# Kernel optimization log

Hardware: AMD Instinct MI355X
Metric: run time of the kernel (lower is better)

The kernel has to match this reference:

```python
import jax, jax.numpy as jnp
import numpy as np

B, N, K = 4, 50000, 128   # batch, surface points, deformation nodes
GD = 128                  # SDF grid resolution (D=H=W)


def setup_inputs() -> dict:
    key = jax.random.key(0)
    ks = jax.random.split(key, 7)
    constants = jax.random.normal(ks[0], (B, K), dtype=jnp.float32)
    scales = 0.05 + 0.25 * jax.random.uniform(ks[1], (B, K), dtype=jnp.float32)
    # proper-ish rotations via QR of random matrices
    M = jax.random.normal(ks[2], (B, K, 3, 3), dtype=jnp.float32)
    rotations, _ = jnp.linalg.qr(M)
    centers = jax.random.uniform(ks[3], (B, K, 3), dtype=jnp.float32, minval=-0.5, maxval=0.5)
    surface_samples = jax.random.uniform(ks[4], (B, N, 6), dtype=jnp.float32, minval=-0.5, maxval=0.5)
    grid = jax.random.normal(ks[5], (B, GD, GD, GD), dtype=jnp.float32)
    # world2grid maps world [-0.5,0.5] -> grid index [0, GD-1]
    w2g = np.zeros((B, 4, 4), dtype=np.float32)
    w2g[:, 0, 0] = w2g[:, 1, 1] = w2g[:, 2, 2] = float(GD - 1)
    w2g[:, :3, 3] = float(GD - 1) / 2.0
    w2g[:, 3, 3] = 1.0
    world2grid = jnp.asarray(w2g)
    return {"constants": constants, "scales": scales, "rotations": rotations,
            "centers": centers, "surface_samples": surface_samples,
            "grid": grid, "world2grid": world2grid}


def _trilinear_border(vol, xyz):
    """torch grid_sample (5D, bilinear, align_corners=True, border) for one batch.
    vol: (D,H,W); xyz: (N,3) normalized coords in [-1,1], order (x,y,z)."""
    D, H, W = vol.shape
    x = jnp.clip((xyz[:, 0] + 1.0) * 0.5 * (W - 1), 0.0, W - 1)
    y = jnp.clip((xyz[:, 1] + 1.0) * 0.5 * (H - 1), 0.0, H - 1)
    z = jnp.clip((xyz[:, 2] + 1.0) * 0.5 * (D - 1), 0.0, D - 1)
    x0 = jnp.floor(x); y0 = jnp.floor(y); z0 = jnp.floor(z)
    fx = x - x0; fy = y - y0; fz = z - z0
    x0i = x0.astype(jnp.int32); x1i = jnp.minimum(x0i + 1, W - 1)
    y0i = y0.astype(jnp.int32); y1i = jnp.minimum(y0i + 1, H - 1)
    z0i = z0.astype(jnp.int32); z1i = jnp.minimum(z0i + 1, D - 1)
    c000 = vol[z0i, y0i, x0i]; c001 = vol[z0i, y0i, x1i]
    c010 = vol[z0i, y1i, x0i]; c011 = vol[z0i, y1i, x1i]
    c100 = vol[z1i, y0i, x0i]; c101 = vol[z1i, y0i, x1i]
    c110 = vol[z1i, y1i, x0i]; c111 = vol[z1i, y1i, x1i]
    c00 = c000 * (1 - fx) + c001 * fx
    c01 = c010 * (1 - fx) + c011 * fx
    c10 = c100 * (1 - fx) + c101 * fx
    c11 = c110 * (1 - fx) + c111 * fx
    c0 = c00 * (1 - fy) + c01 * fy
    c1 = c10 * (1 - fy) + c11 * fy
    return c0 * (1 - fz) + c1 * fz


def reference(constants, scales, rotations, centers, surface_samples, grid, world2grid):
    pts = surface_samples[..., :3]                       # (B,N,3)
    diff = pts[:, :, None, :] - centers[:, None, :, :]   # (B,N,K,3)  == p - t_source
    d2 = jnp.sum(diff * diff, axis=-1)                   # (B,N,K)
    # sample_rbf_weights with use_constants=True
    w = jnp.exp(-d2 / (2.0 * scales * scales)[:, None, :]) * (constants * constants)[:, None, :]
    w = w / jnp.sum(w, axis=-1, keepdims=True)           # normalize over nodes

    # target = roll batch by -1 (source_idx+1 mod B)
    R_t = jnp.roll(rotations, -1, axis=0)
    R_rel = jnp.einsum('bkij,bklj->bkil', R_t, rotations)       # R_target @ R_source^T
    c_t = jnp.roll(centers, -1, axis=0)
    transformed = jnp.einsum('bkij,bnkj->bnki', R_rel, diff) + c_t[:, None, :, :]
    blended = jnp.einsum('bnk,bnki->bni', w, transformed)        # (B,N,3)

    w2g_t = jnp.roll(world2grid, -1, axis=0)
    A = w2g_t[:, :3, :3]
    t = w2g_t[:, :3, 3]
    gcs = jnp.einsum('bij,bnj->bni', A, blended) + t[:, None, :]  # grid coords (x,y,z)

    D, H, W = grid.shape[1], grid.shape[2], grid.shape[3]
    denom = jnp.array([W - 1, H - 1, D - 1], dtype=gcs.dtype)
    gcs = 2.0 * (gcs / denom) - 1.0                               # normalize to [-1,1]

    grid_t = jnp.roll(grid, -1, axis=0)
    sdf = jax.vmap(_trilinear_border)(grid_t, gcs)                # (B,N)
    return jnp.sum(jnp.mean(sdf * sdf, axis=1))
```

## Files before the change

kernel.cpp:

```cpp
#include <hip/hip_runtime.h>
#include <stdint.h>

#define K_   128
#define GD_  128
#define PSTR 20
#define KPW  32

typedef float v2f __attribute__((ext_vector_type(2)));

static __device__ __forceinline__ float fast_exp2(float x) {
#if __has_builtin(__builtin_amdgcn_exp2f)
    return __builtin_amdgcn_exp2f(x);
#else
    return exp2f(x);
#endif
}

static __device__ __forceinline__ v2f vfma(v2f a, v2f b, v2f c) {
    return __builtin_elementwise_fma(a, b, c);
}
static __device__ __forceinline__ v2f vfma_s(float a, v2f b, v2f c) {
    return __builtin_elementwise_fma((v2f)(a), b, c);
}

__global__ void surf_param_kernel(
    const float* __restrict__ constants,
    const float* __restrict__ scales,
    const float* __restrict__ rotations,
    const float* __restrict__ centers,
    const float* __restrict__ w2g,
    float* __restrict__ params,
    float* __restrict__ out,
    int B)
{
    int idx = blockIdx.x * blockDim.x + threadIdx.x;
    if (idx == 0) out[0] = 0.0f;
    if (idx >= B * K_) return;
    int b = idx / K_, k = idx - b * K_;
    int bn = (b + 1 == B) ? 0 : (b + 1);
    const float L2E = 1.4426950408889634f;

    const float* R  = rotations + (size_t)(b  * K_ + k) * 9;
    const float* Rt = rotations + (size_t)(bn * K_ + k) * 9;
    float m[9];
#pragma unroll
    for (int i = 0; i < 3; ++i)
#pragma unroll
        for (int l = 0; l < 3; ++l)
            m[i * 3 + l] = Rt[i * 3 + 0] * R[l * 3 + 0]
                         + Rt[i * 3 + 1] * R[l * 3 + 1]
                         + Rt[i * 3 + 2] * R[l * 3 + 2];

    const float* Aw = w2g + (size_t)bn * 16;
    float G[9], A[9] = {Aw[0], Aw[1], Aw[2], Aw[4], Aw[5], Aw[6], Aw[8], Aw[9], Aw[10]};
    float T[3] = {Aw[3], Aw[7], Aw[11]};
#pragma unroll
    for (int i = 0; i < 3; ++i)
#pragma unroll
        for (int l = 0; l < 3; ++l)
            G[i * 3 + l] = A[i * 3 + 0] * m[0 * 3 + l]
                         + A[i * 3 + 1] * m[1 * 3 + l]
                         + A[i * 3 + 2] * m[2 * 3 + l];

    const float* c  = centers + (size_t)(b  * K_ + k) * 3;
    const float* ct = centers + (size_t)(bn * K_ + k) * 3;
    float c0 = c[0], c1 = c[1], c2 = c[2];
    float vw0 = ct[0] - (m[0] * c0 + m[1] * c1 + m[2] * c2);
    float vw1 = ct[1] - (m[3] * c0 + m[4] * c1 + m[5] * c2);
    float vw2 = ct[2] - (m[6] * c0 + m[7] * c1 + m[8] * c2);
    float v0 = A[0] * vw0 + A[1] * vw1 + A[2] * vw2 + T[0];
    float v1 = A[3] * vw0 + A[4] * vw1 + A[5] * vw2 + T[1];
    float v2 = A[6] * vw0 + A[7] * vw1 + A[8] * vw2 + T[2];

    float sig = scales[b * K_ + k];
    float s   = 1.0f / (2.0f * sig * sig);
    float con = constants[b * K_ + k];
    float s2n = -s * L2E;
    float r   = log2f(con * con) + s2n * (c0 * c0 + c1 * c1 + c2 * c2);

    float* o = params + (size_t)idx * PSTR;
    o[0] = G[0]; o[1] = G[1]; o[2] = G[2]; o[3] = G[3];
    o[4] = G[4]; o[5] = G[5]; o[6] = G[6]; o[7] = G[7];
    o[8] = G[8]; o[9] = v0;  o[10] = v1;  o[11] = v2;
    o[12] = -2.0f * s2n * c0;
    o[13] = -2.0f * s2n * c1;
    o[14] = -2.0f * s2n * c2;
    o[15] = r;
    o[16] = s2n;
    o[17] = 0.f; o[18] = 0.f; o[19] = 0.f;
}

__global__ __launch_bounds__(256) void surf_loss_kernel(
    const float* __restrict__ sp,
    const float* __restrict__ grid,
    const float* __restrict__ params,
    float* __restrict__ out,
    int N, int B, int bpb)
{
    __shared__ float4 lds_part[4 * 4 * 64];
    __shared__ float  red[4];

    const int tid  = threadIdx.x;
    const int lane = tid & 63;
    const int wave = tid >> 6;
    const int blk  = blockIdx.x;
    const int b    = blk / bpb;
    const int base = (blk - b * bpb) * 256;
    const int bn   = (b + 1 == B) ? 0 : (b + 1);

    v2f px2[2], py2[2], pz2[2], pq2[2];
    v2f ax2[2], ay2[2], az2[2], aw2[2];
    const float* spb = sp + (size_t)b * N * 6;
#pragma unroll
    for (int j = 0; j < 4; ++j) {
        int n = base + j * 64 + lane;
        int nn = (n < N) ? n : 0;
        const float* q = spb + (size_t)nn * 6;
        float x = q[0], y = q[1], z = q[2];
        px2[j >> 1][j & 1] = x;
        py2[j >> 1][j & 1] = y;
        pz2[j >> 1][j & 1] = z;
        pq2[j >> 1][j & 1] = x * x + y * y + z * z;
    }
#pragma unroll
    for (int g = 0; g < 2; ++g) {
        ax2[g] = (v2f)0.f; ay2[g] = (v2f)0.f; az2[g] = (v2f)0.f; aw2[g] = (v2f)0.f;
    }

    const int k0 = __builtin_amdgcn_readfirstlane(wave * KPW);
    const float* __restrict__ pb = params + (size_t)b * K_ * PSTR + (size_t)k0 * PSTR;

#pragma unroll 2
    for (int kk = 0; kk < KPW; ++kk) {
        const float* pk = pb + kk * PSTR;
        const float4 f0 = *(const float4*)(pk + 0);
        const float4 f1 = *(const float4*)(pk + 4);
        const float4 f2 = *(const float4*)(pk + 8);
        const float4 f3 = *(const float4*)(pk + 12);
        const float  s2 = pk[16];
#pragma unroll
        for (int g = 0; g < 2; ++g) {
            v2f e = vfma_s(s2, pq2[g],
                    vfma_s(f3.z, pz2[g],
                    vfma_s(f3.y, py2[g],
                    vfma_s(f3.x, px2[g], (v2f)(f3.w)))));
            v2f w2;
            w2.x = fast_exp2(e.x);
            w2.y = fast_exp2(e.y);
            v2f tx = vfma_s(f0.x, px2[g],
                     vfma_s(f0.y, py2[g],
                     vfma_s(f0.z, pz2[g], (v2f)(f2.y))));
            v2f ty = vfma_s(f0.w, px2[g],
                     vfma_s(f1.x, py2[g],
                     vfma_s(f1.y, pz2[g], (v2f)(f2.z))));
            v2f tz = vfma_s(f1.z, px2[g],
                     vfma_s(f1.w, py2[g],
                     vfma_s(f2.x, pz2[g], (v2f)(f2.w))));
            ax2[g] = vfma(w2, tx, ax2[g]);
            ay2[g] = vfma(w2, ty, ay2[g]);
            az2[g] = vfma(w2, tz, az2[g]);
            aw2[g] += w2;
        }
    }

#pragma unroll
    for (int j = 0; j < 4; ++j)
        lds_part[((wave * 4 + j) << 6) + lane] =
            make_float4(ax2[j >> 1][j & 1], ay2[j >> 1][j & 1],
                        az2[j >> 1][j & 1], aw2[j >> 1][j & 1]);
    __syncthreads();

    float accum = 0.0f;
    {
        int n = base + wave * 64 + lane;
        if (n < N) {
            float sx = 0.f, sy = 0.f, sz = 0.f, sw = 0.f;
#pragma unroll
            for (int w = 0; w < 4; ++w) {
                float4 t = lds_part[((w * 4 + wave) << 6) + lane];
                sx += t.x; sy += t.y; sz += t.z; sw += t.w;
            }
            float inv = 1.0f / sw;
            float x = fminf(fmaxf(sx * inv, 0.0f), (float)(GD_ - 1));
            float y = fminf(fmaxf(sy * inv, 0.0f), (float)(GD_ - 1));
            float z = fminf(fmaxf(sz * inv, 0.0f), (float)(GD_ - 1));
            float x0f = floorf(x), y0f = floorf(y), z0f = floorf(z);
            float fx = x - x0f, fy = y - y0f, fz = z - z0f;
            int x0 = (int)x0f, y0 = (int)y0f, z0 = (int)z0f;
            int x1 = x0 + 1 > GD_ - 1 ? GD_ - 1 : x0 + 1;
            int y1 = y0 + 1 > GD_ - 1 ? GD_ - 1 : y0 + 1;
            int z1 = z0 + 1 > GD_ - 1 ? GD_ - 1 : z0 + 1;
            const float* gb = grid + (size_t)bn * GD_ * GD_ * GD_;
            int zy00 = (z0 * GD_ + y0) * GD_;
            int zy01 = (z0 * GD_ + y1) * GD_;
            int zy10 = (z1 * GD_ + y0) * GD_;
            int zy11 = (z1 * GD_ + y1) * GD_;
            float c000 = gb[zy00 + x0], c001 = gb[zy00 + x1];
            float c010 = gb[zy01 + x0], c011 = gb[zy01 + x1];
            float c100 = gb[zy10 + x0], c101 = gb[zy10 + x1];
            float c110 = gb[zy11 + x0], c111 = gb[zy11 + x1];
            float ofx = 1.0f - fx, ofy = 1.0f - fy, ofz = 1.0f - fz;
            float c00 = c000 * ofx + c001 * fx;
            float c01 = c010 * ofx + c011 * fx;
            float c10 = c100 * ofx + c101 * fx;
            float c11 = c110 * ofx + c111 * fx;
            float c0 = c00 * ofy + c01 * fy;
            float c1 = c10 * ofy + c11 * fy;
            float sdf = c0 * ofz + c1 * fz;
            accum = sdf * sdf;
        }
    }

#pragma unroll
    for (int off = 32; off > 0; off >>= 1)
        accum += __shfl_down(accum, off, 64);
    if (lane == 0) red[wave] = accum;
    __syncthreads();
    if (tid == 0)
        atomicAdd(out, (red[0] + red[1] + red[2] + red[3]) * (1.0f / (float)N));
}

extern "C" void kernel_launch(void* const* d_in, const int* in_sizes, int n_in,
                              void* d_out, int out_size, void* d_ws, size_t ws_size,
                              hipStream_t stream) {
    const float* constants = (const float*)d_in[0];
    const float* scales    = (const float*)d_in[1];
    const float* rotations = (const float*)d_in[2];
    const float* centers   = (const float*)d_in[3];
    const float* sp        = (const float*)d_in[4];
    const float* grid      = (const float*)d_in[5];
    const float* w2g       = (const float*)d_in[6];
    float* out = (float*)d_out;
    float* params = (float*)d_ws;

    const int B = in_sizes[6] / 16;
    const int N = in_sizes[4] / (6 * B);

    int np = B * K_;
    hipLaunchKernelGGL(surf_param_kernel, dim3((np + 255) / 256), dim3(256), 0, stream,
                       constants, scales, rotations, centers, w2g, params, out, B);

    const int bpb = (N + 255) / 256;
    hipLaunchKernelGGL(surf_loss_kernel, dim3(B * bpb), dim3(256), 0, stream,
                       sp, grid, params, out, N, B, bpb);
}
```

Baseline: 111.3 us.

## Fuse per-node parameter precompute into loss kernel via shared memory

Removes the separate parameter kernel and global workspace. Each block of the loss kernel now computes the 128 node parameters for its batch into LDS, then reads them from LDS in the inner loop. A tiny kernel zeroes the output. This trades a kernel launch and a global round trip for redundant per-block recomputation (about 782 blocks) and an extra barrier. Parameter reads also move from scalar or broadcast global loads to LDS loads.

```diff
diff --git a/kernel.cpp b/kernel.cpp
--- a/kernel.cpp
+++ b/kernel.cpp
@@ -23,80 +23,20 @@
     return __builtin_elementwise_fma((v2f)(a), b, c);
 }
 
-__global__ void surf_param_kernel(
+__global__ void zero_out_kernel(float* __restrict__ out) { out[0] = 0.0f; }
+
+__global__ __launch_bounds__(256) void surf_fused_kernel(
     const float* __restrict__ constants,
     const float* __restrict__ scales,
     const float* __restrict__ rotations,
     const float* __restrict__ centers,
-    const float* __restrict__ w2g,
-    float* __restrict__ params,
-    float* __restrict__ out,
-    int B)
-{
-    int idx = blockIdx.x * blockDim.x + threadIdx.x;
-    if (idx == 0) out[0] = 0.0f;
-    if (idx >= B * K_) return;
-    int b = idx / K_, k = idx - b * K_;
-    int bn = (b + 1 == B) ? 0 : (b + 1);
-    const float L2E = 1.4426950408889634f;
-
-    const float* R  = rotations + (size_t)(b  * K_ + k) * 9;
-    const float* Rt = rotations + (size_t)(bn * K_ + k) * 9;
-    float m[9];
-#pragma unroll
-    for (int i = 0; i < 3; ++i)
-#pragma unroll
-        for (int l = 0; l < 3; ++l)
-            m[i * 3 + l] = Rt[i * 3 + 0] * R[l * 3 + 0]
-                         + Rt[i * 3 + 1] * R[l * 3 + 1]
-                         + Rt[i * 3 + 2] * R[l * 3 + 2];
-
-    const float* Aw = w2g + (size_t)bn * 16;
-    float G[9], A[9] = {Aw[0], Aw[1], Aw[2], Aw[4], Aw[5], Aw[6], Aw[8], Aw[9], Aw[10]};
-    float T[3] = {Aw[3], Aw[7], Aw[11]};
-#pragma unroll
-    for (int i = 0; i < 3; ++i)
-#pragma unroll
-        for (int l = 0; l < 3; ++l)
-            G[i * 3 + l] = A[i * 3 + 0] * m[0 * 3 + l]
-                         + A[i * 3 + 1] * m[1 * 3 + l]
-                         + A[i * 3 + 2] * m[2 * 3 + l];
-
-    const float* c  = centers + (size_t)(b  * K_ + k) * 3;
-    const float* ct = centers + (size_t)(bn * K_ + k) * 3;
-    float c0 = c[0], c1 = c[1], c2 = c[2];
-    float vw0 = ct[0] - (m[0] * c0 + m[1] * c1 + m[2] * c2);
-    float vw1 = ct[1] - (m[3] * c0 + m[4] * c1 + m[5] * c2);
-    float vw2 = ct[2] - (m[6] * c0 + m[7] * c1 + m[8] * c2);
-    float v0 = A[0] * vw0 + A[1] * vw1 + A[2] * vw2 + T[0];
-    float v1 = A[3] * vw0 + A[4] * vw1 + A[5] * vw2 + T[1];
-    float v2 = A[6] * vw0 + A[7] * vw1 + A[8] * vw2 + T[2];
-
-    float sig = scales[b * K_ + k];
-    float s   = 1.0f / (2.0f * sig * sig);
-    float con = constants[b * K_ + k];
-    float s2n = -s * L2E;
-    float r   = log2f(con * con) + s2n * (c0 * c0 + c1 * c1 + c2 * c2);
-
-    float* o = params + (size_t)idx * PSTR;
-    o[0] = G[0]; o[1] = G[1]; o[2] = G[2]; o[3] = G[3];
-    o[4] = G[4]; o[5] = G[5]; o[6] = G[6]; o[7] = G[7];
-    o[8] = G[8]; o[9] = v0;  o[10] = v1;  o[11] = v2;
-    o[12] = -2.0f * s2n * c0;
-    o[13] = -2.0f * s2n * c1;
-    o[14] = -2.0f * s2n * c2;
-    o[15] = r;
-    o[16] = s2n;
-    o[17] = 0.f; o[18] = 0.f; o[19] = 0.f;
-}
-
-__global__ __launch_bounds__(256) void surf_loss_kernel(
     const float* __restrict__ sp,
     const float* __restrict__ grid,
-    const float* __restrict__ params,
+    const float* __restrict__ w2g,
     float* __restrict__ out,
     int N, int B, int bpb)
 {
+    __shared__ float  lds_par[K_ * PSTR];
     __shared__ float4 lds_part[4 * 4 * 64];
     __shared__ float  red[4];
 
@@ -127,17 +67,70 @@
         ax2[g] = (v2f)0.f; ay2[g] = (v2f)0.f; az2[g] = (v2f)0.f; aw2[g] = (v2f)0.f;
     }
 
-    const int k0 = __builtin_amdgcn_readfirstlane(wave * KPW);
-    const float* __restrict__ pb = params + (size_t)b * K_ * PSTR + (size_t)k0 * PSTR;
-
+    if (tid < K_) {
+        const int k = tid;
+        const float L2E = 1.4426950408889634f;
+
+        const float* R  = rotations + (size_t)(b  * K_ + k) * 9;
+        const float* Rt = rotations + (size_t)(bn * K_ + k) * 9;
+        float m[9];
+#pragma unroll
+        for (int i = 0; i < 3; ++i)
+#pragma unroll
+            for (int l = 0; l < 3; ++l)
+                m[i * 3 + l] = Rt[i * 3 + 0] * R[l * 3 + 0]
+                             + Rt[i * 3 + 1] * R[l * 3 + 1]
+                             + Rt[i * 3 + 2] * R[l * 3 + 2];
+
+        const float* Aw = w2g + (size_t)bn * 16;
+        float G[9], A[9] = {Aw[0], Aw[1], Aw[2], Aw[4], Aw[5], Aw[6], Aw[8], Aw[9], Aw[10]};
+        float T[3] = {Aw[3], Aw[7], Aw[11]};
+#pragma unroll
+        for (int i = 0; i < 3; ++i)
+#pragma unroll
+            for (int l = 0; l < 3; ++l)
+                G[i * 3 + l] = A[i * 3 + 0] * m[0 * 3 + l]
+                             + A[i * 3 + 1] * m[1 * 3 + l]
+                             + A[i * 3 + 2] * m[2 * 3 + l];
+
+        const float* c  = centers + (size_t)(b  * K_ + k) * 3;
+        const float* ct = centers + (size_t)(bn * K_ + k) * 3;
+        float c0 = c[0], c1 = c[1], c2 = c[2];
+        float vw0 = ct[0] - (m[0] * c0 + m[1] * c1 + m[2] * c2);
+        float vw1 = ct[1] - (m[3] * c0 + m[4] * c1 + m[5] * c2);
+        float vw2 = ct[2] - (m[6] * c0 + m[7] * c1 + m[8] * c2);
+        float v0 = A[0] * vw0 + A[1] * vw1 + A[2] * vw2 + T[0];
+        float v1 = A[3] * vw0 + A[4] * vw1 + A[5] * vw2 + T[1];
+        float v2 = A[6] * vw0 + A[7] * vw1 + A[8] * vw2 + T[2];
+
+        float sig = scales[b * K_ + k];
+        float s   = 1.0f / (2.0f * sig * sig);
+        float con = constants[b * K_ + k];
+        float s2n = -s * L2E;
+        float r   = log2f(con * con) + s2n * (c0 * c0 + c1 * c1 + c2 * c2);
+
+        float* o = lds_par + (size_t)k * PSTR;
+        o[0] = G[0]; o[1] = G[1]; o[2] = G[2]; o[3] = G[3];
+        o[4] = G[4]; o[5] = G[5]; o[6] = G[6]; o[7] = G[7];
+        o[8] = G[8]; o[9] = v0;  o[10] = v1;  o[11] = v2;
+        o[12] = -2.0f * s2n * c0;
+        o[13] = -2.0f * s2n * c1;
+        o[14] = -2.0f * s2n * c2;
+        o[15] = r;
+        o[16] = s2n;
+        o[17] = 0.f; o[18] = 0.f; o[19] = 0.f;
+    }
+    __syncthreads();
+
+    const int k0 = wave * KPW;
 #pragma unroll 2
     for (int kk = 0; kk < KPW; ++kk) {
-        const float* pk = pb + kk * PSTR;
-        const float4 f0 = *(const float4*)(pk + 0);
-        const float4 f1 = *(const float4*)(pk + 4);
-        const float4 f2 = *(const float4*)(pk + 8);
-        const float4 f3 = *(const float4*)(pk + 12);
-        const float  s2 = pk[16];
+        const float4* f = (const float4*)(lds_par + (k0 + kk) * PSTR);
+        const float4 f0 = f[0];
+        const float4 f1 = f[1];
+        const float4 f2 = f[2];
+        const float4 f3 = f[3];
+        const float  s2 = lds_par[(k0 + kk) * PSTR + 16];
 #pragma unroll
         for (int g = 0; g < 2; ++g) {
             v2f e = vfma_s(s2, pq2[g],
@@ -231,16 +224,14 @@
     const float* grid      = (const float*)d_in[5];
     const float* w2g       = (const float*)d_in[6];
     float* out = (float*)d_out;
-    float* params = (float*)d_ws;
 
     const int B = in_sizes[6] / 16;
     const int N = in_sizes[4] / (6 * B);
 
-    int np = B * K_;
-    hipLaunchKernelGGL(surf_param_kernel, dim3((np + 255) / 256), dim3(256), 0, stream,
-                       constants, scales, rotations, centers, w2g, params, out, B);
+    hipLaunchKernelGGL(zero_out_kernel, dim3(1), dim3(1), 0, stream, out);
 
     const int bpb = (N + 255) / 256;
-    hipLaunchKernelGGL(surf_loss_kernel, dim3(B * bpb), dim3(256), 0, stream,
-                       sp, grid, params, out, N, B, bpb);
-}
+    hipLaunchKernelGGL(surf_fused_kernel, dim3(B * bpb), dim3(256), 0, stream,
+                       constants, scales, rotations, centers, sp, grid, w2g,
+                       out, N, B, bpb);
+}
```

New measurement: 106.7 us, median of 2. 4.1% less time.
